# Kernel tuning notes

Hardware: AMD Instinct MI355X
Metric: run time of the kernel (lower is better)

The kernel has to match this reference:

```python
import jax, jax.numpy as jnp
import numpy as np
import math

B, T, C = 4, 2048, 1024
H = 16
D_FF = 4 * C


def new_gelu(x):
    # tanh-approx GELU, identical to the torch.jit.script version
    return 0.5 * x * (1.0 + jnp.tanh(math.sqrt(2.0 / math.pi) * (x + 0.044715 * x ** 3)))


def layernorm(x, g, b, eps=1e-5):
    mu = jnp.mean(x, axis=-1, keepdims=True)
    var = jnp.var(x, axis=-1, keepdims=True)
    return (x - mu) * jax.lax.rsqrt(var + eps) * g + b


def setup_inputs() -> dict:
    key = jax.random.key(0)
    ks = jax.random.split(key, 8)
    s = 0.02
    return {
        "x": jax.random.normal(ks[0], (B, T, C), dtype=jnp.float32),
        "ln1_g": jnp.ones((C,), jnp.float32),
        "ln1_b": jnp.zeros((C,), jnp.float32),
        "w_qkv": jax.random.normal(ks[1], (C, 3 * C), jnp.float32) * s,
        "b_qkv": jnp.zeros((3 * C,), jnp.float32),
        "w_attnproj": jax.random.normal(ks[2], (C, C), jnp.float32) * s,
        "b_attnproj": jnp.zeros((C,), jnp.float32),
        "ln2_g": jnp.ones((C,), jnp.float32),
        "ln2_b": jnp.zeros((C,), jnp.float32),
        "w_fc": jax.random.normal(ks[3], (C, D_FF), jnp.float32) * s,
        "b_fc": jnp.zeros((D_FF,), jnp.float32),
        "w_proj": jax.random.normal(ks[4], (D_FF, C), jnp.float32) * s,
        "b_proj": jnp.zeros((C,), jnp.float32),
    }


def _block(x, ln1_g, ln1_b, w_qkv, b_qkv, w_attnproj, b_attnproj,
           ln2_g, ln2_b, w_fc, b_fc, w_proj, b_proj):
    # --- self-attention (pre-LN, non-causal, dropout=0) ---
    h = layernorm(x, ln1_g, ln1_b)
    qkv = h @ w_qkv + b_qkv                       # [B,T,3C]
    q, k, v = jnp.split(qkv, 3, axis=-1)
    hd = C // H
    q = q.reshape(B, T, H, hd).transpose(0, 2, 1, 3)  # [B,H,T,hd]
    k = k.reshape(B, T, H, hd).transpose(0, 2, 1, 3)
    v = v.reshape(B, T, H, hd).transpose(0, 2, 1, 3)
    att = jnp.einsum('bhqd,bhkd->bhqk', q, k) * (1.0 / math.sqrt(hd))
    att = jax.nn.softmax(att, axis=-1)
    y = jnp.einsum('bhqk,bhkd->bhqd', att, v)
    y = y.transpose(0, 2, 1, 3).reshape(B, T, C)
    x = x + (y @ w_attnproj + b_attnproj)
    # --- MLP ---
    h = layernorm(x, ln2_g, ln2_b)
    h = new_gelu(h @ w_fc + b_fc)
    x = x + (h @ w_proj + b_proj)
    return x


def reference(x, ln1_g, ln1_b, w_qkv, b_qkv, w_attnproj, b_attnproj,
              ln2_g, ln2_b, w_fc, b_fc, w_proj, b_proj):
    return _block(x, ln1_g, ln1_b, w_qkv, b_qkv, w_attnproj, b_attnproj,
                  ln2_g, ln2_b, w_fc, b_fc, w_proj, b_proj)
```

## Files before the change

kernel.cpp:

```cpp
#include <hip/hip_runtime.h>


typedef __attribute__((ext_vector_type(8))) short short8;
typedef __attribute__((ext_vector_type(4))) float fx4;

__device__ __forceinline__ unsigned short f2bf(float f) {
    union { float f; unsigned u; } v; v.f = f;
    unsigned r = v.u + 0x7fffu + ((v.u >> 16) & 1u);
    return (unsigned short)(r >> 16);
}

__device__ __forceinline__ unsigned pack_trunc(float lo, float hi) {
    return __builtin_amdgcn_perm(__float_as_uint(hi), __float_as_uint(lo),
                                 0x07060302u);
}

__device__ __forceinline__ void ld_lds16(const void* g, void* l) {
    __builtin_amdgcn_global_load_lds(
        (const __attribute__((address_space(1))) unsigned int*)g,
        (__attribute__((address_space(3))) unsigned int*)l, 16, 0, 0);
}

__global__ __launch_bounds__(256) void transpose_to_bf16(
    const float* __restrict__ in, unsigned short* __restrict__ out, int R, int Cn)
{
    __shared__ float tile[32][33];
    int c0 = blockIdx.x * 32, r0 = blockIdx.y * 32;
    int tx = threadIdx.x, ty = threadIdx.y;
    for (int i = 0; i < 4; ++i)
        tile[ty + i * 8][tx] = in[(size_t)(r0 + ty + i * 8) * Cn + c0 + tx];
    __syncthreads();
    for (int i = 0; i < 4; ++i)
        out[(size_t)(c0 + ty + i * 8) * R + r0 + tx] = f2bf(tile[tx][ty + i * 8]);
}

__global__ __launch_bounds__(256) void layernorm_bf16(
    const float* __restrict__ x, const float* __restrict__ g,
    const float* __restrict__ bb, unsigned short* __restrict__ out)
{
    const int C = 1024;
    int row = blockIdx.x;
    const float* xr = x + (size_t)row * C;
    float4 v = ((const float4*)xr)[threadIdx.x];
    float s  = v.x + v.y + v.z + v.w;
    float ss = v.x * v.x + v.y * v.y + v.z * v.z + v.w * v.w;
    for (int off = 32; off >= 1; off >>= 1) {
        s  += __shfl_xor(s,  off);
        ss += __shfl_xor(ss, off);
    }
    __shared__ float sbuf[2][4];
    int wave = threadIdx.x >> 6;
    if ((threadIdx.x & 63) == 0) { sbuf[0][wave] = s; sbuf[1][wave] = ss; }
    __syncthreads();
    s  = sbuf[0][0] + sbuf[0][1] + sbuf[0][2] + sbuf[0][3];
    ss = sbuf[1][0] + sbuf[1][1] + sbuf[1][2] + sbuf[1][3];
    float mu   = s * (1.0f / C);
    float var  = ss * (1.0f / C) - mu * mu;
    float rstd = rsqrtf(var + 1e-5f);
    int i = threadIdx.x * 4;
    ushort4 o;
    o.x = f2bf((v.x - mu) * rstd * g[i + 0] + bb[i + 0]);
    o.y = f2bf((v.y - mu) * rstd * g[i + 1] + bb[i + 1]);
    o.z = f2bf((v.z - mu) * rstd * g[i + 2] + bb[i + 2]);
    o.w = f2bf((v.w - mu) * rstd * g[i + 3] + bb[i + 3]);
    ((ushort4*)(out + (size_t)row * C))[threadIdx.x] = o;
}

template <int EPI>
__global__ __launch_bounds__(256) void gemm_bt(
    const unsigned short* __restrict__ A, const unsigned short* __restrict__ Bt,
    const float* __restrict__ bias, const float* __restrict__ resid,
    void* __restrict__ out0, void* __restrict__ out1, void* __restrict__ out2,
    int M, int N, int K)
{
    __shared__ unsigned short As[128 * 32];
    __shared__ unsigned short Bs[128 * 32];
    const int bm = blockIdx.y * 128, bn = blockIdx.x * 128;
    const int t = threadIdx.x, wave = t >> 6, lane = t & 63;
    const int wm = (wave >> 1) * 64, wn = (wave & 1) * 64;
    const int lq = lane >> 4, lr = lane & 15;

    fx4 acc[4][4];
    for (int mi = 0; mi < 4; ++mi)
        for (int ni = 0; ni < 4; ++ni)
            acc[mi][ni] = 0.0f;

    for (int k0 = 0; k0 < K; k0 += 32) {
        #pragma unroll
        for (int c = 0; c < 2; ++c) {
            int idx = t + c * 256;
            int row = idx >> 2, ps = idx & 3;
            int p = (ps - (row >> 1)) & 3;
            ld_lds16(&A[(size_t)(bm + row) * K + k0 + p * 8], &As[idx * 8]);
            ld_lds16(&Bt[(size_t)(bn + row) * K + k0 + p * 8], &Bs[idx * 8]);
        }
        __syncthreads();
        short8 af[4], bfr[4];
        #pragma unroll
        for (int mi = 0; mi < 4; ++mi) {
            int row = wm + mi * 16 + lr;
            af[mi] = *(const short8*)&As[row * 32 + (((lq + (row >> 1)) & 3) << 3)];
        }
        #pragma unroll
        for (int ni = 0; ni < 4; ++ni) {
            int row = wn + ni * 16 + lr;
            bfr[ni] = *(const short8*)&Bs[row * 32 + (((lq + (row >> 1)) & 3) << 3)];
        }
        #pragma unroll
        for (int mi = 0; mi < 4; ++mi)
            #pragma unroll
            for (int ni = 0; ni < 4; ++ni)
                acc[mi][ni] = __builtin_amdgcn_mfma_f32_16x16x32_bf16(
                    af[mi], bfr[ni], acc[mi][ni], 0, 0, 0);
        __syncthreads();
    }

    #pragma unroll
    for (int mi = 0; mi < 4; ++mi) {
        #pragma unroll
        for (int ni = 0; ni < 4; ++ni) {
            int col = bn + wn + ni * 16 + lr;
            float bcol = bias[col];
            #pragma unroll
            for (int r = 0; r < 4; ++r) {
                int row = bm + wm + mi * 16 + lq * 4 + r;
                float v = acc[mi][ni][r] + bcol;
                if constexpr (EPI == 0) {
                    int sec = col >> 10, cc = col & 1023;
                    int head = cc >> 6, d = cc & 63;
                    int batch = row >> 11, tt = row & 2047;
                    size_t bh = (size_t)(batch * 16 + head);
                    if (sec == 0)
                        ((unsigned short*)out0)[(bh * 2048 + tt) * 64 + d] = f2bf(v);
                    else if (sec == 1)
                        ((unsigned short*)out1)[(bh * 2048 + tt) * 64 + d] = f2bf(v);
                    else
                        ((unsigned short*)out2)[(bh * 64 + d) * 2048 + tt] = f2bf(v);
                } else if constexpr (EPI == 1) {
                    ((float*)out0)[(size_t)row * N + col] =
                        resid[(size_t)row * N + col] + v;
                } else {
                    float u2 = 1.5957691216057308f * (v + 0.044715f * v * v * v);
                    float gl = v / (1.0f + __expf(-u2));
                    ((unsigned short*)out0)[(size_t)row * N + col] = f2bf(gl);
                }
            }
        }
    }
}

__global__ __launch_bounds__(256) void flash_attn(
    const unsigned short* __restrict__ Q, const unsigned short* __restrict__ Kk,
    const unsigned short* __restrict__ Vt, unsigned short* __restrict__ Y)
{
    __shared__ unsigned short Ks[64 * 72];
    __shared__ unsigned short Vs[64 * 72];
    __shared__ unsigned short Ps[4][16 * 72];
    const int bh = blockIdx.y;
    const int batch = bh >> 4, head = bh & 15;
    const int t = threadIdx.x, w = t >> 6, lane = t & 63;
    const int lq = lane >> 4, lr = lane & 15;
    const int q0 = blockIdx.x * 128 + w * 32;
    const size_t base = (size_t)bh * 2048 * 64;

    short8 qf[2][2];
    #pragma unroll
    for (int qt = 0; qt < 2; ++qt)
        #pragma unroll
        for (int c = 0; c < 2; ++c)
            qf[qt][c] = *(const short8*)
                &Q[base + (size_t)(q0 + qt * 16 + lr) * 64 + c * 32 + lq * 8];

    float l[2] = {0.0f, 0.0f};
    fx4 o[2][4];
    #pragma unroll
    for (int qt = 0; qt < 2; ++qt)
        #pragma unroll
        for (int dn = 0; dn < 4; ++dn) o[qt][dn] = 0.0f;

    for (int kt = 0; kt < 32; ++kt) {
        int kb = kt * 64;
        __syncthreads();
        #pragma unroll
        for (int c = 0; c < 2; ++c) {
            int idx = t + c * 256;
            int row = idx >> 3, col8 = (idx & 7) << 3;
            *(short8*)&Ks[row * 72 + col8] =
                *(const short8*)&Kk[base + (size_t)(kb + row) * 64 + col8];
            *(short8*)&Vs[row * 72 + col8] =
                *(const short8*)&Vt[base + (size_t)row * 2048 + kb + col8];
        }
        __syncthreads();

        #pragma unroll
        for (int qt = 0; qt < 2; ++qt) {
            #pragma unroll
            for (int kn = 0; kn < 4; ++kn) {
                fx4 s = 0.0f;
                #pragma unroll
                for (int c = 0; c < 2; ++c) {
                    short8 kf = *(const short8*)
                        &Ks[(kn * 16 + lr) * 72 + c * 32 + lq * 8];
                    s = __builtin_amdgcn_mfma_f32_16x16x32_bf16(
                        kf, qf[qt][c], s, 0, 0, 0);
                }
                float p0 = __expf(s[0] * 0.125f);
                float p1 = __expf(s[1] * 0.125f);
                float p2 = __expf(s[2] * 0.125f);
                float p3 = __expf(s[3] * 0.125f);
                l[qt] += (p0 + p1) + (p2 + p3);
                uint2 pk;
                pk.x = pack_trunc(p0, p1);
                pk.y = pack_trunc(p2, p3);
                *(uint2*)&Ps[w][lr * 72 + kn * 16 + lq * 4] = pk;
            }
            short8 pf[2];
            #pragma unroll
            for (int c = 0; c < 2; ++c)
                pf[c] = *(const short8*)&Ps[w][lr * 72 + c * 32 + lq * 8];
            #pragma unroll
            for (int dn = 0; dn < 4; ++dn)
                #pragma unroll
                for (int c = 0; c < 2; ++c) {
                    short8 vf = *(const short8*)
                        &Vs[(dn * 16 + lr) * 72 + c * 32 + lq * 8];
                    o[qt][dn] = __builtin_amdgcn_mfma_f32_16x16x32_bf16(
                        vf, pf[c], o[qt][dn], 0, 0, 0);
                }
        }
    }

    #pragma unroll
    for (int qt = 0; qt < 2; ++qt) {
        float ls = l[qt];
        ls += __shfl_xor(ls, 16);
        ls += __shfl_xor(ls, 32);
        float inv = 1.0f / ls;
        int qg = q0 + qt * 16 + lr;
        #pragma unroll
        for (int dn = 0; dn < 4; ++dn) {
            ushort4 ov;
            ov.x = f2bf(o[qt][dn][0] * inv);
            ov.y = f2bf(o[qt][dn][1] * inv);
            ov.z = f2bf(o[qt][dn][2] * inv);
            ov.w = f2bf(o[qt][dn][3] * inv);
            *(ushort4*)&Y[((size_t)(batch * 2048 + qg)) * 1024 +
                          head * 64 + dn * 16 + lq * 4] = ov;
        }
    }
}

extern "C" void kernel_launch(void* const* d_in, const int* in_sizes, int n_in,
                              void* d_out, int out_size, void* d_ws, size_t ws_size,
                              hipStream_t stream)
{
    const float* x      = (const float*)d_in[0];
    const float* ln1_g  = (const float*)d_in[1];
    const float* ln1_b  = (const float*)d_in[2];
    const float* w_qkv  = (const float*)d_in[3];
    const float* b_qkv  = (const float*)d_in[4];
    const float* w_ap   = (const float*)d_in[5];
    const float* b_ap   = (const float*)d_in[6];
    const float* ln2_g  = (const float*)d_in[7];
    const float* ln2_b  = (const float*)d_in[8];
    const float* w_fc   = (const float*)d_in[9];
    const float* b_fc   = (const float*)d_in[10];
    const float* w_proj = (const float*)d_in[11];
    const float* b_proj = (const float*)d_in[12];
    float* out = (float*)d_out;

    char* ws = (char*)d_ws;
    unsigned short* wT_qkv = (unsigned short*)(ws + 0);
    unsigned short* wT_ap  = (unsigned short*)(ws + 6291456);
    unsigned short* wT_fc  = (unsigned short*)(ws + 8388608);
    unsigned short* wT_pr  = (unsigned short*)(ws + 16777216);
    float*          x2     = (float*)(ws + 25165824);
    unsigned short* Abuf   = (unsigned short*)(ws + 58720256);
    unsigned short* Qb     = (unsigned short*)(ws + 75497472);
    unsigned short* Kb     = (unsigned short*)(ws + 75497472 + 16777216);
    unsigned short* Vtb    = (unsigned short*)(ws + 75497472 + 33554432);
    unsigned short* H3     = (unsigned short*)(ws + 75497472);

    dim3 tb(32, 8);
    transpose_to_bf16<<<dim3(3072 / 32, 1024 / 32), tb, 0, stream>>>(w_qkv, wT_qkv, 1024, 3072);
    transpose_to_bf16<<<dim3(1024 / 32, 1024 / 32), tb, 0, stream>>>(w_ap,  wT_ap,  1024, 1024);
    transpose_to_bf16<<<dim3(4096 / 32, 1024 / 32), tb, 0, stream>>>(w_fc,  wT_fc,  1024, 4096);
    transpose_to_bf16<<<dim3(1024 / 32, 4096 / 32), tb, 0, stream>>>(w_proj, wT_pr, 4096, 1024);

    layernorm_bf16<<<8192, 256, 0, stream>>>(x, ln1_g, ln1_b, Abuf);
    gemm_bt<0><<<dim3(24, 64), 256, 0, stream>>>(Abuf, wT_qkv, b_qkv, nullptr,
                                                 Qb, Kb, Vtb, 8192, 3072, 1024);
    flash_attn<<<dim3(16, 64), 256, 0, stream>>>(Qb, Kb, Vtb, Abuf);
    gemm_bt<1><<<dim3(8, 64), 256, 0, stream>>>(Abuf, wT_ap, b_ap, x,
                                                x2, nullptr, nullptr, 8192, 1024, 1024);
    layernorm_bf16<<<8192, 256, 0, stream>>>(x2, ln2_g, ln2_b, Abuf);
    gemm_bt<2><<<dim3(32, 64), 256, 0, stream>>>(Abuf, wT_fc, b_fc, nullptr,
                                                 H3, nullptr, nullptr, 8192, 4096, 1024);
    gemm_bt<1><<<dim3(8, 64), 256, 0, stream>>>(H3, wT_pr, b_proj, x2,
                                                out, nullptr, nullptr, 8192, 1024, 4096);
}
```

Measured before the change: 634.6 us.

## Deepen GEMM K-tile, fold softmax scale into Q, compute row sums via MFMA

The GEMM now stages a 64-wide K slice per iteration with an 8-way XOR swizzle, which halves the number of barrier pairs per output tile. The attention kernel loads K/V tiles through direct global-to-LDS loads with the same swizzle and hoists K/V fragments out of the query loop. Q is pre-scaled by log2(e)/sqrt(d) in the QKV epilogue so the kernel can use a native exp2, and the softmax row sum is taken with an MFMA against a ones vector instead of scalar adds and shuffles. The row sum is now built from the bf16-truncated probabilities, a small accuracy change, and launch bounds request 3 blocks per CU, which may increase register pressure.

Result: faster. 542.4 us (-14.5%).

```diff
diff --git a/kernel.cpp b/kernel.cpp
--- a/kernel.cpp
+++ b/kernel.cpp
@@ -8,6 +8,14 @@
     union { float f; unsigned u; } v; v.f = f;
     unsigned r = v.u + 0x7fffu + ((v.u >> 16) & 1u);
     return (unsigned short)(r >> 16);
+}
+
+__device__ __forceinline__ float fexp2(float x) {
+#if __has_builtin(__builtin_amdgcn_exp2f)
+    return __builtin_amdgcn_exp2f(x);
+#else
+    return __expf(x * 0.69314718055994531f);
+#endif
 }
 
 __device__ __forceinline__ unsigned pack_trunc(float lo, float hi) {
@@ -73,8 +81,8 @@
     void* __restrict__ out0, void* __restrict__ out1, void* __restrict__ out2,
     int M, int N, int K)
 {
-    __shared__ unsigned short As[128 * 32];
-    __shared__ unsigned short Bs[128 * 32];
+    __shared__ unsigned short As[128 * 64];
+    __shared__ unsigned short Bs[128 * 64];
     const int bm = blockIdx.y * 128, bn = blockIdx.x * 128;
     const int t = threadIdx.x, wave = t >> 6, lane = t & 63;
     const int wm = (wave >> 1) * 64, wn = (wave & 1) * 64;
@@ -85,33 +93,38 @@
         for (int ni = 0; ni < 4; ++ni)
             acc[mi][ni] = 0.0f;
 
-    for (int k0 = 0; k0 < K; k0 += 32) {
-        #pragma unroll
-        for (int c = 0; c < 2; ++c) {
+    for (int k0 = 0; k0 < K; k0 += 64) {
+        #pragma unroll
+        for (int c = 0; c < 4; ++c) {
             int idx = t + c * 256;
-            int row = idx >> 2, ps = idx & 3;
-            int p = (ps - (row >> 1)) & 3;
+            int row = idx >> 3, ps = idx & 7;
+            int p = (ps - row) & 7;
             ld_lds16(&A[(size_t)(bm + row) * K + k0 + p * 8], &As[idx * 8]);
             ld_lds16(&Bt[(size_t)(bn + row) * K + k0 + p * 8], &Bs[idx * 8]);
         }
         __syncthreads();
-        short8 af[4], bfr[4];
-        #pragma unroll
-        for (int mi = 0; mi < 4; ++mi) {
-            int row = wm + mi * 16 + lr;
-            af[mi] = *(const short8*)&As[row * 32 + (((lq + (row >> 1)) & 3) << 3)];
-        }
-        #pragma unroll
-        for (int ni = 0; ni < 4; ++ni) {
-            int row = wn + ni * 16 + lr;
-            bfr[ni] = *(const short8*)&Bs[row * 32 + (((lq + (row >> 1)) & 3) << 3)];
-        }
-        #pragma unroll
-        for (int mi = 0; mi < 4; ++mi)
-            #pragma unroll
-            for (int ni = 0; ni < 4; ++ni)
-                acc[mi][ni] = __builtin_amdgcn_mfma_f32_16x16x32_bf16(
-                    af[mi], bfr[ni], acc[mi][ni], 0, 0, 0);
+        #pragma unroll
+        for (int half = 0; half < 2; ++half) {
+            short8 af[4], bfr[4];
+            #pragma unroll
+            for (int mi = 0; mi < 4; ++mi) {
+                int row = wm + mi * 16 + lr;
+                af[mi] = *(const short8*)
+                    &As[row * 64 + (((half * 4 + lq + row) & 7) << 3)];
+            }
+            #pragma unroll
+            for (int ni = 0; ni < 4; ++ni) {
+                int row = wn + ni * 16 + lr;
+                bfr[ni] = *(const short8*)
+                    &Bs[row * 64 + (((half * 4 + lq + row) & 7) << 3)];
+            }
+            #pragma unroll
+            for (int mi = 0; mi < 4; ++mi)
+                #pragma unroll
+                for (int ni = 0; ni < 4; ++ni)
+                    acc[mi][ni] = __builtin_amdgcn_mfma_f32_16x16x32_bf16(
+                        af[mi], bfr[ni], acc[mi][ni], 0, 0, 0);
+        }
         __syncthreads();
     }
 
@@ -131,7 +144,8 @@
                     int batch = row >> 11, tt = row & 2047;
                     size_t bh = (size_t)(batch * 16 + head);
                     if (sec == 0)
-                        ((unsigned short*)out0)[(bh * 2048 + tt) * 64 + d] = f2bf(v);
+                        ((unsigned short*)out0)[(bh * 2048 + tt) * 64 + d] =
+                            f2bf(v * 0.18033688011112042f);
                     else if (sec == 1)
                         ((unsigned short*)out1)[(bh * 2048 + tt) * 64 + d] = f2bf(v);
                     else
@@ -149,12 +163,12 @@
     }
 }
 
-__global__ __launch_bounds__(256) void flash_attn(
+__global__ __launch_bounds__(256, 3) void flash_attn(
     const unsigned short* __restrict__ Q, const unsigned short* __restrict__ Kk,
     const unsigned short* __restrict__ Vt, unsigned short* __restrict__ Y)
 {
-    __shared__ unsigned short Ks[64 * 72];
-    __shared__ unsigned short Vs[64 * 72];
+    __shared__ unsigned short Ks[64 * 64];
+    __shared__ unsigned short Vs[64 * 64];
     __shared__ unsigned short Ps[4][16 * 72];
     const int bh = blockIdx.y;
     const int batch = bh >> 4, head = bh & 15;
@@ -171,71 +185,87 @@
             qf[qt][c] = *(const short8*)
                 &Q[base + (size_t)(q0 + qt * 16 + lr) * 64 + c * 32 + lq * 8];
 
-    float l[2] = {0.0f, 0.0f};
+    short8 ones;
+    #pragma unroll
+    for (int i = 0; i < 8; ++i) ones[i] = (short)0x3F80;
+
+    fx4 lacc[2];
     fx4 o[2][4];
     #pragma unroll
-    for (int qt = 0; qt < 2; ++qt)
+    for (int qt = 0; qt < 2; ++qt) {
+        lacc[qt] = 0.0f;
         #pragma unroll
         for (int dn = 0; dn < 4; ++dn) o[qt][dn] = 0.0f;
+    }
 
     for (int kt = 0; kt < 32; ++kt) {
         int kb = kt * 64;
         __syncthreads();
         #pragma unroll
-        for (int c = 0; c < 2; ++c) {
-            int idx = t + c * 256;
-            int row = idx >> 3, col8 = (idx & 7) << 3;
-            *(short8*)&Ks[row * 72 + col8] =
-                *(const short8*)&Kk[base + (size_t)(kb + row) * 64 + col8];
-            *(short8*)&Vs[row * 72 + col8] =
-                *(const short8*)&Vt[base + (size_t)row * 2048 + kb + col8];
+        for (int c2 = 0; c2 < 2; ++c2) {
+            int idx = t + c2 * 256;
+            int row = idx >> 3, ps = idx & 7;
+            int p = (ps - row) & 7;
+            ld_lds16(&Kk[base + (size_t)(kb + row) * 64 + p * 8], &Ks[idx * 8]);
+            ld_lds16(&Vt[base + (size_t)row * 2048 + kb + p * 8], &Vs[idx * 8]);
         }
         __syncthreads();
+
+        short8 kf[4][2], vf[4][2];
+        #pragma unroll
+        for (int kn = 0; kn < 4; ++kn)
+            #pragma unroll
+            for (int c = 0; c < 2; ++c) {
+                int row = kn * 16 + lr;
+                kf[kn][c] = *(const short8*)
+                    &Ks[row * 64 + (((c * 4 + lq + row) & 7) << 3)];
+            }
+        #pragma unroll
+        for (int dn = 0; dn < 4; ++dn)
+            #pragma unroll
+            for (int c = 0; c < 2; ++c) {
+                int row = dn * 16 + lr;
+                vf[dn][c] = *(const short8*)
+                    &Vs[row * 64 + (((c * 4 + lq + row) & 7) << 3)];
+            }
 
         #pragma unroll
         for (int qt = 0; qt < 2; ++qt) {
             #pragma unroll
             for (int kn = 0; kn < 4; ++kn) {
                 fx4 s = 0.0f;
-                #pragma unroll
-                for (int c = 0; c < 2; ++c) {
-                    short8 kf = *(const short8*)
-                        &Ks[(kn * 16 + lr) * 72 + c * 32 + lq * 8];
-                    s = __builtin_amdgcn_mfma_f32_16x16x32_bf16(
-                        kf, qf[qt][c], s, 0, 0, 0);
-                }
-                float p0 = __expf(s[0] * 0.125f);
-                float p1 = __expf(s[1] * 0.125f);
-                float p2 = __expf(s[2] * 0.125f);
-                float p3 = __expf(s[3] * 0.125f);
-                l[qt] += (p0 + p1) + (p2 + p3);
+                s = __builtin_amdgcn_mfma_f32_16x16x32_bf16(
+                    kf[kn][0], qf[qt][0], s, 0, 0, 0);
+                s = __builtin_amdgcn_mfma_f32_16x16x32_bf16(
+                    kf[kn][1], qf[qt][1], s, 0, 0, 0);
+                float p0 = fexp2(s[0]);
+                float p1 = fexp2(s[1]);
+                float p2 = fexp2(s[2]);
+                float p3 = fexp2(s[3]);
                 uint2 pk;
                 pk.x = pack_trunc(p0, p1);
                 pk.y = pack_trunc(p2, p3);
                 *(uint2*)&Ps[w][lr * 72 + kn * 16 + lq * 4] = pk;
             }
-            short8 pf[2];
-            #pragma unroll
-            for (int c = 0; c < 2; ++c)
-                pf[c] = *(const short8*)&Ps[w][lr * 72 + c * 32 + lq * 8];
-            #pragma unroll
-            for (int dn = 0; dn < 4; ++dn)
-                #pragma unroll
-                for (int c = 0; c < 2; ++c) {
-                    short8 vf = *(const short8*)
-                        &Vs[(dn * 16 + lr) * 72 + c * 32 + lq * 8];
-                    o[qt][dn] = __builtin_amdgcn_mfma_f32_16x16x32_bf16(
-                        vf, pf[c], o[qt][dn], 0, 0, 0);
-                }
+            short8 pf0 = *(const short8*)&Ps[w][lr * 72 + lq * 8];
+            short8 pf1 = *(const short8*)&Ps[w][lr * 72 + 32 + lq * 8];
+            lacc[qt] = __builtin_amdgcn_mfma_f32_16x16x32_bf16(
+                ones, pf0, lacc[qt], 0, 0, 0);
+            lacc[qt] = __builtin_amdgcn_mfma_f32_16x16x32_bf16(
+                ones, pf1, lacc[qt], 0, 0, 0);
+            #pragma unroll
+            for (int dn = 0; dn < 4; ++dn) {
+                o[qt][dn] = __builtin_amdgcn_mfma_f32_16x16x32_bf16(
+                    vf[dn][0], pf0, o[qt][dn], 0, 0, 0);
+                o[qt][dn] = __builtin_amdgcn_mfma_f32_16x16x32_bf16(
+                    vf[dn][1], pf1, o[qt][dn], 0, 0, 0);
+            }
         }
     }
 
     #pragma unroll
     for (int qt = 0; qt < 2; ++qt) {
-        float ls = l[qt];
-        ls += __shfl_xor(ls, 16);
-        ls += __shfl_xor(ls, 32);
-        float inv = 1.0f / ls;
+        float inv = 1.0f / lacc[qt][0];
         int qg = q0 + qt * 16 + lr;
         #pragma unroll
         for (int dn = 0; dn < 4; ++dn) {
```
